# Optimization experiments

Hardware: AMD Instinct MI355X
Metric: run time of the kernel (lower is better)

Reference implementation:

```python
import jax, jax.numpy as jnp
import numpy as np

N_NODES = 50000
N_EDGES = 800000
D_IN = 128
D_HID = 128
D_OUT = 128


def _gcn_layer(x, W, b, src, dst, norm):
    # dense projection then edge-weighted gather -> scatter-add at dst
    h = x @ W                                   # [N, d_out]
    msg = h[src] * norm[:, None]                # [E, d_out]
    out = jax.ops.segment_sum(msg, dst, num_segments=N_NODES)
    return out + b


def setup_inputs() -> dict:
    key = jax.random.key(0)
    k = jax.random.split(key, 8)
    x = jax.random.normal(k[0], (N_NODES, D_IN), dtype=jnp.float32)
    edge_index = jax.random.randint(k[1], (2, N_EDGES), 0, N_NODES, dtype=jnp.int64)
    edge_weight = jax.random.uniform(k[2], (N_EDGES,), dtype=jnp.float32)
    # GCNConv params (glorot-ish scale)
    s1 = 1.0 / np.sqrt(D_IN)
    s2 = 1.0 / np.sqrt(D_HID)
    W1 = jax.random.normal(k[3], (D_IN, D_HID), dtype=jnp.float32) * s1
    b1 = jnp.zeros((D_HID,), dtype=jnp.float32)
    W2 = jax.random.normal(k[4], (D_HID, D_OUT), dtype=jnp.float32) * s2
    b2 = jnp.zeros((D_OUT,), dtype=jnp.float32)
    return {"x": x, "edge_index": edge_index, "edge_weight": edge_weight,
            "W1": W1, "b1": b1, "W2": W2, "b2": b2}


def reference(x, edge_index, edge_weight, W1, b1, W2, b2):
    src, dst = edge_index[0], edge_index[1]
    # gcn_norm (add_self_loops=False): deg from scatter-add of edge_weight at dst
    deg = jax.ops.segment_sum(edge_weight, dst, num_segments=N_NODES)
    dinv = jnp.where(deg > 0, jax.lax.rsqrt(jnp.maximum(deg, 1e-30)), 0.0)
    norm = dinv[src] * edge_weight * dinv[dst]  # [E]
    h = jax.nn.relu(_gcn_layer(x, W1, b1, src, dst, norm))
    out = _gcn_layer(h, W2, b2, src, dst, norm)
    # F.dropout in eval mode (deterministic reference) is identity
    return out
```

## Files before the change

### kernel.cpp

```cpp
#include <hip/hip_runtime.h>

#define N_NODES 50000
#define N_EDGES 800000
#define D 128
#define MAXDEG 64
#define NBUCK 196
#define BUCKCAP 5120
#define EPB 4096
#define NBB 196
#define SP 136

typedef __attribute__((ext_vector_type(8))) short bf16x8;
typedef __attribute__((ext_vector_type(4))) float f32x4;

__device__ inline unsigned short f2bf(float f) {
    unsigned u = __float_as_uint(f);
    unsigned r = (u + 0x7fffu + ((u >> 16) & 1u)) >> 16;
    return (unsigned short)r;
}

__global__ __launch_bounds__(256) void k_bucket(const int* __restrict__ src,
                                                const int* __restrict__ dst,
                                                const float* __restrict__ ew,
                                                int* __restrict__ cursor,
                                                uint2* __restrict__ buck,
                                                const float* __restrict__ W1,
                                                const float* __restrict__ W2,
                                                unsigned short* __restrict__ Wt1,
                                                unsigned short* __restrict__ Wt2) {
    if (blockIdx.x >= NBB) {
        const float* W = (blockIdx.x == NBB) ? W1 : W2;
        unsigned short* Wt = (blockIdx.x == NBB) ? Wt1 : Wt2;
        for (int idx = threadIdx.x; idx < D * D; idx += 256) {
            int n = idx & 127, k = idx >> 7;
            Wt[n * D + k] = f2bf(W[k * D + n]);
        }
        return;
    }
    __shared__ uint2 sorted[EPB];
    __shared__ int hist[NBUCK];
    __shared__ int scn[NBUCK];
    __shared__ int gbase[NBUCK];
    __shared__ int s[256];
    int tid = threadIdx.x;
    int e0 = blockIdx.x * EPB;
    for (int i = tid; i < NBUCK; i += 256) hist[i] = 0;
    __syncthreads();
    #pragma unroll
    for (int j = 0; j < 16; ++j) {
        int e = e0 + j * 256 + tid;
        if (e < N_EDGES) atomicAdd(&hist[dst[e] >> 8], 1);
    }
    __syncthreads();
    int v = tid < NBUCK ? hist[tid] : 0;
    s[tid] = v;
    __syncthreads();
    for (int off = 1; off < 256; off <<= 1) {
        int u = tid >= off ? s[tid - off] : 0;
        __syncthreads();
        s[tid] += u;
        __syncthreads();
    }
    int excl = s[tid] - v;
    if (tid < NBUCK) {
        scn[tid] = excl;
        gbase[tid] = v ? atomicAdd(&cursor[tid], v) : 0;
        hist[tid] = excl;
    }
    __syncthreads();
    #pragma unroll
    for (int j = 0; j < 16; ++j) {
        int e = e0 + j * 256 + tid;
        if (e < N_EDGES) {
            int d = dst[e];
            int sv = src[e];
            unsigned wf = min(__float2uint_rn(ew[e] * 65536.f), 65535u);
            int slot = atomicAdd(&hist[d >> 8], 1);
            sorted[slot] = make_uint2(((unsigned)sv << 16) | wf, (unsigned)d);
        }
    }
    __syncthreads();
    int total = min(EPB, N_EDGES - e0);
    for (int i = tid; i < total; i += 256) {
        uint2 en = sorted[i];
        int bk = (int)(en.y >> 8);
        int g = gbase[bk] + (i - scn[bk]);
        if (g < BUCKCAP)
            buck[(size_t)bk * BUCKCAP + g] = make_uint2(en.x, en.y & 255u);
    }
}

#define GB 782
__global__ __launch_bounds__(256) void k_build_gemm(
        const int* __restrict__ cursor, const uint2* __restrict__ buck,
        unsigned* __restrict__ csr, int* __restrict__ cnt,
        float* __restrict__ dinv,
        const float* __restrict__ X, const unsigned short* __restrict__ Wt1,
        unsigned short* __restrict__ h0) {
    __shared__ union SM {
        struct {
            unsigned csr_loc[256 * MAXDEG];
            int cnt_loc[256];
            int deg_loc[256];
        } b;
        unsigned short sX[64 * D];
    } sm;
    int tid = threadIdx.x;

    if (blockIdx.x < NBUCK) {
        int b = blockIdx.x;
        sm.b.cnt_loc[tid] = 0;
        sm.b.deg_loc[tid] = 0;
        {
            uint4* z4 = (uint4*)sm.b.csr_loc;
            #pragma unroll
            for (int i = 0; i < (256 * MAXDEG / 4) / 256; ++i)
                z4[i * 256 + tid] = make_uint4(0u, 0u, 0u, 0u);
        }
        __syncthreads();
        int n = min(cursor[b], BUCKCAP);
        const uint2* bb = buck + (size_t)b * BUCKCAP;
        for (int i = tid; i < n; i += 256) {
            uint2 e = bb[i];
            int ln = e.y;
            int slot = atomicAdd(&sm.b.cnt_loc[ln], 1);
            if (slot < MAXDEG) sm.b.csr_loc[ln * MAXDEG + slot] = e.x;
            atomicAdd(&sm.b.deg_loc[ln], (int)(e.x & 0xffffu));
        }
        __syncthreads();
        int node0 = b * 256;
        int nnodes = min(256, N_NODES - node0);
        uint4* g = (uint4*)(csr + (size_t)node0 * MAXDEG);
        const uint4* l = (const uint4*)sm.b.csr_loc;
        int nv = nnodes * (MAXDEG / 4);
        for (int i = tid; i < nv; i += 256) g[i] = l[i];
        if (tid < nnodes) {
            int node = node0 + tid;
            cnt[node] = min(sm.b.cnt_loc[tid], MAXDEG);
            float sum = (float)sm.b.deg_loc[tid] * (1.f / 65536.f);
            dinv[node] = sum > 0.f ? rsqrtf(fmaxf(sum, 1e-30f)) : 0.f;
        }
        return;
    }

    int row0 = (blockIdx.x - NBUCK) * 64;
    int nr = min(64, N_NODES - row0);
    {
        const float4* xs = (const float4*)(X + (size_t)row0 * D);
        int nvec = nr * (D / 4);
        for (int i = tid; i < nvec; i += 256) {
            float4 v = xs[i];
            ushort4 o;
            o.x = f2bf(v.x); o.y = f2bf(v.y); o.z = f2bf(v.z); o.w = f2bf(v.w);
            *(ushort4*)(sm.sX + i * 4) = o;
        }
    }
    __syncthreads();

    int wave = tid >> 6, lane = tid & 63;
    int m = lane & 15, quad = lane >> 4;
    f32x4 acc[8];
    #pragma unroll
    for (int i = 0; i < 8; ++i) acc[i] = (f32x4){0.f, 0.f, 0.f, 0.f};

    const unsigned short* aBase = sm.sX + (wave * 16 + m) * D + quad * 8;
    #pragma unroll
    for (int c = 0; c < 4; ++c) {
        bf16x8 a = *(const bf16x8*)(aBase + c * 32);
        #pragma unroll
        for (int n0 = 0; n0 < 8; ++n0) {
            bf16x8 b = *(const bf16x8*)(Wt1 + (n0 * 16 + m) * D + c * 32 + quad * 8);
            acc[n0] = __builtin_amdgcn_mfma_f32_16x16x32_bf16(a, b, acc[n0], 0, 0, 0);
        }
    }

    unsigned short* sOut = sm.sX + wave * 16 * D;
    __syncthreads();
    #pragma unroll
    for (int n0 = 0; n0 < 8; ++n0)
        #pragma unroll
        for (int i = 0; i < 4; ++i)
            sOut[(quad * 4 + i) * D + n0 * 16 + m] = f2bf(acc[n0][i]);
    __syncthreads();
    int rr = lane >> 2, c0 = (lane & 3) * 32;
    int grow = row0 + wave * 16 + rr;
    if (grow < N_NODES) {
        uint4* dstp = (uint4*)(h0 + (size_t)grow * D + c0);
        const uint4* srcp = (const uint4*)(sOut + rr * D + c0);
        dstp[0] = srcp[0]; dstp[1] = srcp[1]; dstp[2] = srcp[2]; dstp[3] = srcp[3];
    }
}

__global__ __launch_bounds__(256) void k_agg_mm(const unsigned short* __restrict__ H,
                                                const int* __restrict__ cnt,
                                                const unsigned* __restrict__ csr,
                                                const float* __restrict__ dinv,
                                                const float* __restrict__ b1,
                                                const unsigned short* __restrict__ Wt2,
                                                unsigned short* __restrict__ Hb) {
    __shared__ unsigned short sT[16 * SP];
    int tid = threadIdx.x, wave = tid >> 6, lane = tid & 63;
    int g = lane >> 4, fl = lane & 15;
    int nb = blockIdx.x * 16;
    int node = nb + wave * 4 + g;

    int end = min(cnt[node], MAXDEG);
    const uint4* row4 = (const uint4*)(csr + (size_t)node * MAXDEG);
    float acc[8] = {0.f, 0.f, 0.f, 0.f, 0.f, 0.f, 0.f, 0.f};
    for (int b0 = 0; b0 < end; b0 += 8) {
        uint4 ca = row4[(b0 >> 2)];
        uint4 cb = row4[(b0 >> 2) + 1];
        unsigned cs[8] = {ca.x, ca.y, ca.z, ca.w, cb.x, cb.y, cb.z, cb.w};
        uint4 u[8];
        float nmv[8];
        #pragma unroll
        for (int j = 0; j < 8; ++j) {
            unsigned sv = cs[j] >> 16;
            u[j] = *(const uint4*)(H + (size_t)sv * D + fl * 8);
            nmv[j] = (float)(cs[j] & 0xffffu) * (1.f / 65536.f) * dinv[sv];
        }
        #pragma unroll
        for (int j = 0; j < 8; ++j) {
            unsigned a0[4] = {u[j].x, u[j].y, u[j].z, u[j].w};
            #pragma unroll
            for (int q = 0; q < 4; ++q) {
                acc[2 * q]     += __uint_as_float(a0[q] << 16) * nmv[j];
                acc[2 * q + 1] += __uint_as_float(a0[q] & 0xffff0000u) * nmv[j];
            }
        }
    }
    {
        float dn = dinv[node];
        int f = fl * 8;
        float4 bv0 = *(const float4*)(b1 + f);
        float4 bv1 = *(const float4*)(b1 + f + 4);
        ushort4 o0, o1;
        o0.x = f2bf(fmaxf(acc[0] * dn + bv0.x, 0.f));
        o0.y = f2bf(fmaxf(acc[1] * dn + bv0.y, 0.f));
        o0.z = f2bf(fmaxf(acc[2] * dn + bv0.z, 0.f));
        o0.w = f2bf(fmaxf(acc[3] * dn + bv0.w, 0.f));
        o1.x = f2bf(fmaxf(acc[4] * dn + bv1.x, 0.f));
        o1.y = f2bf(fmaxf(acc[5] * dn + bv1.y, 0.f));
        o1.z = f2bf(fmaxf(acc[6] * dn + bv1.z, 0.f));
        o1.w = f2bf(fmaxf(acc[7] * dn + bv1.w, 0.f));
        unsigned short* tp = sT + (wave * 4 + g) * SP + f;
        *(ushort4*)(tp) = o0;
        *(ushort4*)(tp + 4) = o1;
    }
    __syncthreads();

    int m = lane & 15, quad = lane >> 4;
    f32x4 acc2[2];
    acc2[0] = (f32x4){0.f, 0.f, 0.f, 0.f};
    acc2[1] = (f32x4){0.f, 0.f, 0.f, 0.f};
    #pragma unroll
    for (int c = 0; c < 4; ++c) {
        bf16x8 a = *(const bf16x8*)(sT + m * SP + c * 32 + quad * 8);
        #pragma unroll
        for (int t = 0; t < 2; ++t) {
            int n0 = wave * 2 + t;
            bf16x8 b = *(const bf16x8*)(Wt2 + (n0 * 16 + m) * D + c * 32 + quad * 8);
            acc2[t] = __builtin_amdgcn_mfma_f32_16x16x32_bf16(a, b, acc2[t], 0, 0, 0);
        }
    }
    float dv[4];
    #pragma unroll
    for (int i = 0; i < 4; ++i) dv[i] = dinv[nb + quad * 4 + i];
    __syncthreads();
    #pragma unroll
    for (int t = 0; t < 2; ++t)
        #pragma unroll
        for (int i = 0; i < 4; ++i)
            sT[(quad * 4 + i) * SP + (wave * 2 + t) * 16 + m] = f2bf(acc2[t][i] * dv[i]);
    __syncthreads();
    int rr = tid >> 4, cc = (tid & 15) * 8;
    *(uint4*)(Hb + (size_t)(nb + rr) * D + cc) = *(const uint4*)(sT + rr * SP + cc);
}

__global__ __launch_bounds__(256) void k_aggregate(const unsigned short* __restrict__ H,
                                                   const int* __restrict__ cnt,
                                                   const unsigned* __restrict__ csr,
                                                   const float* __restrict__ dinv,
                                                   const float* __restrict__ bias,
                                                   float* __restrict__ out) {
    int tid = threadIdx.x, wave = tid >> 6, lane = tid & 63;
    int g = lane >> 4, fl = lane & 15;
    int node = blockIdx.x * 16 + wave * 4 + g;

    int end = min(cnt[node], MAXDEG);
    const uint4* row4 = (const uint4*)(csr + (size_t)node * MAXDEG);
    float acc[8] = {0.f, 0.f, 0.f, 0.f, 0.f, 0.f, 0.f, 0.f};
    for (int b0 = 0; b0 < end; b0 += 8) {
        uint4 ca = row4[(b0 >> 2)];
        uint4 cb = row4[(b0 >> 2) + 1];
        unsigned cs[8] = {ca.x, ca.y, ca.z, ca.w, cb.x, cb.y, cb.z, cb.w};
        uint4 u[8];
        float nmv[8];
        #pragma unroll
        for (int j = 0; j < 8; ++j) {
            unsigned sv = cs[j] >> 16;
            u[j] = *(const uint4*)(H + (size_t)sv * D + fl * 8);
            nmv[j] = (float)(cs[j] & 0xffffu) * (1.f / 65536.f);
        }
        #pragma unroll
        for (int j = 0; j < 8; ++j) {
            unsigned a0[4] = {u[j].x, u[j].y, u[j].z, u[j].w};
            #pragma unroll
            for (int q = 0; q < 4; ++q) {
                acc[2 * q]     += __uint_as_float(a0[q] << 16) * nmv[j];
                acc[2 * q + 1] += __uint_as_float(a0[q] & 0xffff0000u) * nmv[j];
            }
        }
    }
    float dn = dinv[node];
    int f = fl * 8;
    float4 bv0 = *(const float4*)(bias + f);
    float4 bv1 = *(const float4*)(bias + f + 4);
    float* op = out + (size_t)node * D + f;
    *(float4*)(op) = make_float4(acc[0] * dn + bv0.x, acc[1] * dn + bv0.y,
                                 acc[2] * dn + bv0.z, acc[3] * dn + bv0.w);
    *(float4*)(op + 4) = make_float4(acc[4] * dn + bv1.x, acc[5] * dn + bv1.y,
                                     acc[6] * dn + bv1.z, acc[7] * dn + bv1.w);
}

extern "C" void kernel_launch(void* const* d_in, const int* in_sizes, int n_in,
                              void* d_out, int out_size, void* d_ws, size_t ws_size,
                              hipStream_t stream) {
    const float* x   = (const float*)d_in[0];
    const int*   ei  = (const int*)d_in[1];
    const float* ew  = (const float*)d_in[2];
    const float* W1  = (const float*)d_in[3];
    const float* b1  = (const float*)d_in[4];
    const float* W2  = (const float*)d_in[5];
    const float* b2  = (const float*)d_in[6];
    float* out = (float*)d_out;

    const int* src = ei;
    const int* dst = ei + N_EDGES;

    char* base = (char*)d_ws;
    size_t off = 0;
    auto take = [&](size_t bytes) -> char* {
        char* p = base + off;
        off += (bytes + 255) & ~(size_t)255;
        return p;
    };
    int*      cursor = (int*)take(NBUCK * 4);
    size_t zero_bytes = off;
    float*    dinv = (float*)take(N_NODES * 4);
    int*      cnt  = (int*)take(N_NODES * 4);
    uint2*    buck = (uint2*)take((size_t)NBUCK * BUCKCAP * 8);
    unsigned* csr  = (unsigned*)take((size_t)N_NODES * MAXDEG * 4);
    unsigned short* Wt1 = (unsigned short*)take(D * D * 2);
    unsigned short* Wt2 = (unsigned short*)take(D * D * 2);
    unsigned short* h0  = (unsigned short*)take((size_t)N_NODES * D * 2);
    unsigned short* hb  = (unsigned short*)take((size_t)N_NODES * D * 2);

    hipMemsetAsync(d_ws, 0, zero_bytes, stream);

    const int FB = N_NODES / 16;
    const int AB = N_NODES / 16;

    k_bucket<<<NBB + 2, 256, 0, stream>>>(src, dst, ew, cursor, buck,
                                          W1, W2, Wt1, Wt2);
    k_build_gemm<<<NBUCK + GB, 256, 0, stream>>>(cursor, buck, csr, cnt, dinv,
                                                 x, Wt1, h0);
    k_agg_mm<<<FB, 256, 0, stream>>>(h0, cnt, csr, dinv, b1, Wt2, hb);
    k_aggregate<<<AB, 256, 0, stream>>>(hb, cnt, csr, dinv, b2, out);
}
```

Before: 194.9 us.

## Replace two-pass bucket sort CSR build with direct global-atomic CSR insertion

Drops the shared-memory bucket sort and the per-bucket build pass. Each edge now inserts itself into the padded CSR with global atomics on cnt and deg. The memset is replaced by a zeroing kernel that also does the weight transposes, and dinv is computed from the integer degree inside the consumers rather than stored. This removes one intermediate buffer pass and the bucket scratch, but puts many scattered global atomics and uncoalesced CSR writes in its place, and it must zero the whole CSR region (about 12.8MB) every call.

```diff
diff --git a/kernel.cpp b/kernel.cpp
--- a/kernel.cpp
+++ b/kernel.cpp
@@ -4,11 +4,11 @@
 #define N_EDGES 800000
 #define D 128
 #define MAXDEG 64
-#define NBUCK 196
-#define BUCKCAP 5120
-#define EPB 4096
-#define NBB 196
 #define SP 136
+
+#define EB 391
+#define GB 782
+#define PZB 200
 
 typedef __attribute__((ext_vector_type(8))) short bf16x8;
 typedef __attribute__((ext_vector_type(4))) float f32x4;
@@ -19,131 +19,68 @@
     return (unsigned short)r;
 }
 
-__global__ __launch_bounds__(256) void k_bucket(const int* __restrict__ src,
-                                                const int* __restrict__ dst,
-                                                const float* __restrict__ ew,
-                                                int* __restrict__ cursor,
-                                                uint2* __restrict__ buck,
-                                                const float* __restrict__ W1,
-                                                const float* __restrict__ W2,
-                                                unsigned short* __restrict__ Wt1,
-                                                unsigned short* __restrict__ Wt2) {
-    if (blockIdx.x >= NBB) {
-        const float* W = (blockIdx.x == NBB) ? W1 : W2;
-        unsigned short* Wt = (blockIdx.x == NBB) ? Wt1 : Wt2;
-        for (int idx = threadIdx.x; idx < D * D; idx += 256) {
+__device__ inline float deg2dinv(int di) {
+    return di > 0 ? rsqrtf((float)di * (1.f / 65536.f)) : 0.f;
+}
+
+__global__ __launch_bounds__(256) void k_prep(const float* __restrict__ W1,
+                                              const float* __restrict__ W2,
+                                              unsigned short* __restrict__ Wt1,
+                                              unsigned short* __restrict__ Wt2,
+                                              uint4* __restrict__ zbase,
+                                              int nz4) {
+    int tid = threadIdx.x;
+    if (blockIdx.x < 2) {
+        const float* W = (blockIdx.x == 0) ? W1 : W2;
+        unsigned short* Wt = (blockIdx.x == 0) ? Wt1 : Wt2;
+        for (int idx = tid; idx < D * D; idx += 256) {
             int n = idx & 127, k = idx >> 7;
             Wt[n * D + k] = f2bf(W[k * D + n]);
         }
         return;
     }
-    __shared__ uint2 sorted[EPB];
-    __shared__ int hist[NBUCK];
-    __shared__ int scn[NBUCK];
-    __shared__ int gbase[NBUCK];
-    __shared__ int s[256];
-    int tid = threadIdx.x;
-    int e0 = blockIdx.x * EPB;
-    for (int i = tid; i < NBUCK; i += 256) hist[i] = 0;
-    __syncthreads();
-    #pragma unroll
-    for (int j = 0; j < 16; ++j) {
-        int e = e0 + j * 256 + tid;
-        if (e < N_EDGES) atomicAdd(&hist[dst[e] >> 8], 1);
-    }
-    __syncthreads();
-    int v = tid < NBUCK ? hist[tid] : 0;
-    s[tid] = v;
-    __syncthreads();
-    for (int off = 1; off < 256; off <<= 1) {
-        int u = tid >= off ? s[tid - off] : 0;
-        __syncthreads();
-        s[tid] += u;
-        __syncthreads();
-    }
-    int excl = s[tid] - v;
-    if (tid < NBUCK) {
-        scn[tid] = excl;
-        gbase[tid] = v ? atomicAdd(&cursor[tid], v) : 0;
-        hist[tid] = excl;
-    }
-    __syncthreads();
-    #pragma unroll
-    for (int j = 0; j < 16; ++j) {
-        int e = e0 + j * 256 + tid;
-        if (e < N_EDGES) {
-            int d = dst[e];
-            int sv = src[e];
-            unsigned wf = min(__float2uint_rn(ew[e] * 65536.f), 65535u);
-            int slot = atomicAdd(&hist[d >> 8], 1);
-            sorted[slot] = make_uint2(((unsigned)sv << 16) | wf, (unsigned)d);
-        }
-    }
-    __syncthreads();
-    int total = min(EPB, N_EDGES - e0);
-    for (int i = tid; i < total; i += 256) {
-        uint2 en = sorted[i];
-        int bk = (int)(en.y >> 8);
-        int g = gbase[bk] + (i - scn[bk]);
-        if (g < BUCKCAP)
-            buck[(size_t)bk * BUCKCAP + g] = make_uint2(en.x, en.y & 255u);
-    }
-}
-
-#define GB 782
-__global__ __launch_bounds__(256) void k_build_gemm(
-        const int* __restrict__ cursor, const uint2* __restrict__ buck,
-        unsigned* __restrict__ csr, int* __restrict__ cnt,
-        float* __restrict__ dinv,
+    for (int i = (blockIdx.x - 2) * 256 + tid; i < nz4; i += PZB * 256)
+        zbase[i] = make_uint4(0u, 0u, 0u, 0u);
+}
+
+__global__ __launch_bounds__(256) void k_csr_gemm(
+        const int* __restrict__ src, const int* __restrict__ dst,
+        const float* __restrict__ ew,
+        int* __restrict__ cnt, int* __restrict__ deg,
+        unsigned* __restrict__ csr,
         const float* __restrict__ X, const unsigned short* __restrict__ Wt1,
         unsigned short* __restrict__ h0) {
-    __shared__ union SM {
-        struct {
-            unsigned csr_loc[256 * MAXDEG];
-            int cnt_loc[256];
-            int deg_loc[256];
-        } b;
-        unsigned short sX[64 * D];
-    } sm;
+    __shared__ unsigned short sX[64 * D];
     int tid = threadIdx.x;
 
-    if (blockIdx.x < NBUCK) {
-        int b = blockIdx.x;
-        sm.b.cnt_loc[tid] = 0;
-        sm.b.deg_loc[tid] = 0;
-        {
-            uint4* z4 = (uint4*)sm.b.csr_loc;
-            #pragma unroll
-            for (int i = 0; i < (256 * MAXDEG / 4) / 256; ++i)
-                z4[i * 256 + tid] = make_uint4(0u, 0u, 0u, 0u);
-        }
-        __syncthreads();
-        int n = min(cursor[b], BUCKCAP);
-        const uint2* bb = buck + (size_t)b * BUCKCAP;
-        for (int i = tid; i < n; i += 256) {
-            uint2 e = bb[i];
-            int ln = e.y;
-            int slot = atomicAdd(&sm.b.cnt_loc[ln], 1);
-            if (slot < MAXDEG) sm.b.csr_loc[ln * MAXDEG + slot] = e.x;
-            atomicAdd(&sm.b.deg_loc[ln], (int)(e.x & 0xffffu));
-        }
-        __syncthreads();
-        int node0 = b * 256;
-        int nnodes = min(256, N_NODES - node0);
-        uint4* g = (uint4*)(csr + (size_t)node0 * MAXDEG);
-        const uint4* l = (const uint4*)sm.b.csr_loc;
-        int nv = nnodes * (MAXDEG / 4);
-        for (int i = tid; i < nv; i += 256) g[i] = l[i];
-        if (tid < nnodes) {
-            int node = node0 + tid;
-            cnt[node] = min(sm.b.cnt_loc[tid], MAXDEG);
-            float sum = (float)sm.b.deg_loc[tid] * (1.f / 65536.f);
-            dinv[node] = sum > 0.f ? rsqrtf(fmaxf(sum, 1e-30f)) : 0.f;
+    if (blockIdx.x < EB) {
+        int e0 = blockIdx.x * 2048;
+        int d8[8];
+        unsigned p8[8];
+        #pragma unroll
+        for (int j = 0; j < 8; ++j) {
+            int e = e0 + j * 256 + tid;
+            if (e < N_EDGES) {
+                d8[j] = dst[e];
+                unsigned wf = min(__float2uint_rn(ew[e] * 65536.f), 65535u);
+                p8[j] = ((unsigned)src[e] << 16) | wf;
+            } else {
+                d8[j] = -1;
+            }
+        }
+        #pragma unroll
+        for (int j = 0; j < 8; ++j) {
+            if (d8[j] >= 0) {
+                int slot = atomicAdd(&cnt[d8[j]], 1);
+                if (slot < MAXDEG)
+                    csr[(size_t)d8[j] * MAXDEG + slot] = p8[j];
+                atomicAdd(&deg[d8[j]], (int)(p8[j] & 0xffffu));
+            }
         }
         return;
     }
 
-    int row0 = (blockIdx.x - NBUCK) * 64;
+    int row0 = (blockIdx.x - EB) * 64;
     int nr = min(64, N_NODES - row0);
     {
         const float4* xs = (const float4*)(X + (size_t)row0 * D);
@@ -152,7 +89,7 @@
             float4 v = xs[i];
             ushort4 o;
             o.x = f2bf(v.x); o.y = f2bf(v.y); o.z = f2bf(v.z); o.w = f2bf(v.w);
-            *(ushort4*)(sm.sX + i * 4) = o;
+            *(ushort4*)(sX + i * 4) = o;
         }
     }
     __syncthreads();
@@ -163,7 +100,7 @@
     #pragma unroll
     for (int i = 0; i < 8; ++i) acc[i] = (f32x4){0.f, 0.f, 0.f, 0.f};
 
-    const unsigned short* aBase = sm.sX + (wave * 16 + m) * D + quad * 8;
+    const unsigned short* aBase = sX + (wave * 16 + m) * D + quad * 8;
     #pragma unroll
     for (int c = 0; c < 4; ++c) {
         bf16x8 a = *(const bf16x8*)(aBase + c * 32);
@@ -174,7 +111,7 @@
         }
     }
 
-    unsigned short* sOut = sm.sX + wave * 16 * D;
+    unsigned short* sOut = sX + wave * 16 * D;
     __syncthreads();
     #pragma unroll
     for (int n0 = 0; n0 < 8; ++n0)
@@ -194,7 +131,7 @@
 __global__ __launch_bounds__(256) void k_agg_mm(const unsigned short* __restrict__ H,
                                                 const int* __restrict__ cnt,
                                                 const unsigned* __restrict__ csr,
-                                                const float* __restrict__ dinv,
+                                                const int* __restrict__ deg,
                                                 const float* __restrict__ b1,
                                                 const unsigned short* __restrict__ Wt2,
                                                 unsigned short* __restrict__ Hb) {
@@ -217,7 +154,8 @@
         for (int j = 0; j < 8; ++j) {
             unsigned sv = cs[j] >> 16;
             u[j] = *(const uint4*)(H + (size_t)sv * D + fl * 8);
-            nmv[j] = (float)(cs[j] & 0xffffu) * (1.f / 65536.f) * dinv[sv];
+            nmv[j] = (float)(cs[j] & 0xffffu) * (1.f / 65536.f)
+                     * deg2dinv(deg[sv]);
         }
         #pragma unroll
         for (int j = 0; j < 8; ++j) {
@@ -230,7 +168,7 @@
         }
     }
     {
-        float dn = dinv[node];
+        float dn = deg2dinv(deg[node]);
         int f = fl * 8;
         float4 bv0 = *(const float4*)(b1 + f);
         float4 bv1 = *(const float4*)(b1 + f + 4);
@@ -265,7 +203,7 @@
     }
     float dv[4];
     #pragma unroll
-    for (int i = 0; i < 4; ++i) dv[i] = dinv[nb + quad * 4 + i];
+    for (int i = 0; i < 4; ++i) dv[i] = deg2dinv(deg[nb + quad * 4 + i]);
     __syncthreads();
     #pragma unroll
     for (int t = 0; t < 2; ++t)
@@ -280,7 +218,7 @@
 __global__ __launch_bounds__(256) void k_aggregate(const unsigned short* __restrict__ H,
                                                    const int* __restrict__ cnt,
                                                    const unsigned* __restrict__ csr,
-                                                   const float* __restrict__ dinv,
+                                                   const int* __restrict__ deg,
                                                    const float* __restrict__ bias,
                                                    float* __restrict__ out) {
     int tid = threadIdx.x, wave = tid >> 6, lane = tid & 63;
@@ -312,7 +250,7 @@
             }
         }
     }
-    float dn = dinv[node];
+    float dn = deg2dinv(deg[node]);
     int f = fl * 8;
     float4 bv0 = *(const float4*)(bias + f);
     float4 bv1 = *(const float4*)(bias + f + 4);
@@ -345,26 +283,24 @@
         off += (bytes + 255) & ~(size_t)255;
         return p;
     };
-    int*      cursor = (int*)take(NBUCK * 4);
-    size_t zero_bytes = off;
-    float*    dinv = (float*)take(N_NODES * 4);
-    int*      cnt  = (int*)take(N_NODES * 4);
-    uint2*    buck = (uint2*)take((size_t)NBUCK * BUCKCAP * 8);
-    unsigned* csr  = (unsigned*)take((size_t)N_NODES * MAXDEG * 4);
+    size_t z0 = off;
+    int*      cnt = (int*)take(N_NODES * 4);
+    int*      deg = (int*)take(N_NODES * 4);
+    unsigned* csr = (unsigned*)take((size_t)N_NODES * MAXDEG * 4);
+    size_t z1 = off;
     unsigned short* Wt1 = (unsigned short*)take(D * D * 2);
     unsigned short* Wt2 = (unsigned short*)take(D * D * 2);
     unsigned short* h0  = (unsigned short*)take((size_t)N_NODES * D * 2);
     unsigned short* hb  = (unsigned short*)take((size_t)N_NODES * D * 2);
 
-    hipMemsetAsync(d_ws, 0, zero_bytes, stream);
+    int nz4 = (int)((z1 - z0) / 16);
 
     const int FB = N_NODES / 16;
-    const int AB = N_NODES / 16;
-
-    k_bucket<<<NBB + 2, 256, 0, stream>>>(src, dst, ew, cursor, buck,
-                                          W1, W2, Wt1, Wt2);
-    k_build_gemm<<<NBUCK + GB, 256, 0, stream>>>(cursor, buck, csr, cnt, dinv,
-                                                 x, Wt1, h0);
-    k_agg_mm<<<FB, 256, 0, stream>>>(h0, cnt, csr, dinv, b1, Wt2, hb);
-    k_aggregate<<<AB, 256, 0, stream>>>(hb, cnt, csr, dinv, b2, out);
-}
+
+    k_prep<<<2 + PZB, 256, 0, stream>>>(W1, W2, Wt1, Wt2,
+                                        (uint4*)(base + z0), nz4);
+    k_csr_gemm<<<EB + GB, 256, 0, stream>>>(src, dst, ew, cnt, deg, csr,
+                                            x, Wt1, h0);
+    k_agg_mm<<<FB, 256, 0, stream>>>(h0, cnt, csr, deg, b1, Wt2, hb);
+    k_aggregate<<<FB, 256, 0, stream>>>(hb, cnt, csr, deg, b2, out);
+}
```

After: 271.3 us. +39.2%, slower.

## Compute degrees globally in bucketing and fold source dinv into GEMM output

Applied to the files above, without the earlier changes.

Degrees are now accumulated with global atomics during the bucketing pass, so dinv can be computed before the first GEMM. The source-side dinv scale is applied to the projected rows instead of being gathered per edge in the aggregation loop. The bucketing pass uses smaller edge chunks (more blocks), and the CSR build splits each 256-node bucket across two blocks, each filtering to its half. The costs are global atomic contention on deg, each half-bucket block reading the full bucket, and an extra deg read in the GEMM epilogue.

```diff
diff --git a/kernel.cpp b/kernel.cpp
--- a/kernel.cpp
+++ b/kernel.cpp
@@ -6,8 +6,10 @@
 #define MAXDEG 64
 #define NBUCK 196
 #define BUCKCAP 5120
-#define EPB 4096
-#define NBB 196
+#define EPB 2048
+#define NBB 391
+#define NB2 392
+#define GB 782
 #define SP 136
 
 typedef __attribute__((ext_vector_type(8))) short bf16x8;
@@ -19,10 +21,15 @@
     return (unsigned short)r;
 }
 
+__device__ inline float deg2dinv(int di) {
+    return di > 0 ? rsqrtf((float)di * (1.f / 65536.f)) : 0.f;
+}
+
 __global__ __launch_bounds__(256) void k_bucket(const int* __restrict__ src,
                                                 const int* __restrict__ dst,
                                                 const float* __restrict__ ew,
                                                 int* __restrict__ cursor,
+                                                int* __restrict__ deg,
                                                 uint2* __restrict__ buck,
                                                 const float* __restrict__ W1,
                                                 const float* __restrict__ W2,
@@ -47,7 +54,7 @@
     for (int i = tid; i < NBUCK; i += 256) hist[i] = 0;
     __syncthreads();
     #pragma unroll
-    for (int j = 0; j < 16; ++j) {
+    for (int j = 0; j < EPB / 256; ++j) {
         int e = e0 + j * 256 + tid;
         if (e < N_EDGES) atomicAdd(&hist[dst[e] >> 8], 1);
     }
@@ -69,12 +76,13 @@
     }
     __syncthreads();
     #pragma unroll
-    for (int j = 0; j < 16; ++j) {
+    for (int j = 0; j < EPB / 256; ++j) {
         int e = e0 + j * 256 + tid;
         if (e < N_EDGES) {
             int d = dst[e];
             int sv = src[e];
             unsigned wf = min(__float2uint_rn(ew[e] * 65536.f), 65535u);
+            atomicAdd(&deg[d], (int)wf);
             int slot = atomicAdd(&hist[d >> 8], 1);
             sorted[slot] = make_uint2(((unsigned)sv << 16) | wf, (unsigned)d);
         }
@@ -90,60 +98,61 @@
     }
 }
 
-#define GB 782
 __global__ __launch_bounds__(256) void k_build_gemm(
         const int* __restrict__ cursor, const uint2* __restrict__ buck,
         unsigned* __restrict__ csr, int* __restrict__ cnt,
-        float* __restrict__ dinv,
+        float* __restrict__ dinv, const int* __restrict__ deg,
         const float* __restrict__ X, const unsigned short* __restrict__ Wt1,
         unsigned short* __restrict__ h0) {
     __shared__ union SM {
         struct {
-            unsigned csr_loc[256 * MAXDEG];
-            int cnt_loc[256];
-            int deg_loc[256];
+            unsigned csr_loc[128 * MAXDEG];
+            int cnt_loc[128];
         } b;
         unsigned short sX[64 * D];
     } sm;
     int tid = threadIdx.x;
 
-    if (blockIdx.x < NBUCK) {
+    if (blockIdx.x < NB2) {
         int b = blockIdx.x;
-        sm.b.cnt_loc[tid] = 0;
-        sm.b.deg_loc[tid] = 0;
+        int bucket = b >> 1;
+        unsigned hbit = (unsigned)(b & 1) << 7;
+        if (tid < 128) sm.b.cnt_loc[tid] = 0;
         {
             uint4* z4 = (uint4*)sm.b.csr_loc;
             #pragma unroll
-            for (int i = 0; i < (256 * MAXDEG / 4) / 256; ++i)
+            for (int i = 0; i < (128 * MAXDEG / 4) / 256; ++i)
                 z4[i * 256 + tid] = make_uint4(0u, 0u, 0u, 0u);
         }
         __syncthreads();
-        int n = min(cursor[b], BUCKCAP);
-        const uint2* bb = buck + (size_t)b * BUCKCAP;
+        int n = min(cursor[bucket], BUCKCAP);
+        const uint2* bb = buck + (size_t)bucket * BUCKCAP;
         for (int i = tid; i < n; i += 256) {
             uint2 e = bb[i];
-            int ln = e.y;
-            int slot = atomicAdd(&sm.b.cnt_loc[ln], 1);
-            if (slot < MAXDEG) sm.b.csr_loc[ln * MAXDEG + slot] = e.x;
-            atomicAdd(&sm.b.deg_loc[ln], (int)(e.x & 0xffffu));
+            if ((e.y & 128u) == hbit) {
+                int ln = (int)(e.y & 127u);
+                int slot = atomicAdd(&sm.b.cnt_loc[ln], 1);
+                if (slot < MAXDEG) sm.b.csr_loc[ln * MAXDEG + slot] = e.x;
+            }
         }
         __syncthreads();
-        int node0 = b * 256;
-        int nnodes = min(256, N_NODES - node0);
-        uint4* g = (uint4*)(csr + (size_t)node0 * MAXDEG);
-        const uint4* l = (const uint4*)sm.b.csr_loc;
-        int nv = nnodes * (MAXDEG / 4);
-        for (int i = tid; i < nv; i += 256) g[i] = l[i];
-        if (tid < nnodes) {
-            int node = node0 + tid;
-            cnt[node] = min(sm.b.cnt_loc[tid], MAXDEG);
-            float sum = (float)sm.b.deg_loc[tid] * (1.f / 65536.f);
-            dinv[node] = sum > 0.f ? rsqrtf(fmaxf(sum, 1e-30f)) : 0.f;
+        int node0 = b * 128;
+        int nnodes = min(128, N_NODES - node0);
+        if (nnodes > 0) {
+            uint4* g = (uint4*)(csr + (size_t)node0 * MAXDEG);
+            const uint4* l = (const uint4*)sm.b.csr_loc;
+            int nv = nnodes * (MAXDEG / 4);
+            for (int i = tid; i < nv; i += 256) g[i] = l[i];
+            if (tid < nnodes) {
+                int node = node0 + tid;
+                cnt[node] = min(sm.b.cnt_loc[tid], MAXDEG);
+                dinv[node] = deg2dinv(deg[node]);
+            }
         }
         return;
     }
 
-    int row0 = (blockIdx.x - NBUCK) * 64;
+    int row0 = (blockIdx.x - NB2) * 64;
     int nr = min(64, N_NODES - row0);
     {
         const float4* xs = (const float4*)(X + (size_t)row0 * D);
@@ -174,13 +183,20 @@
         }
     }
 
+    float dn[4];
+    #pragma unroll
+    for (int i = 0; i < 4; ++i) {
+        int r = row0 + wave * 16 + quad * 4 + i;
+        dn[i] = (r < N_NODES) ? deg2dinv(deg[r]) : 0.f;
+    }
+
     unsigned short* sOut = sm.sX + wave * 16 * D;
     __syncthreads();
     #pragma unroll
     for (int n0 = 0; n0 < 8; ++n0)
         #pragma unroll
         for (int i = 0; i < 4; ++i)
-            sOut[(quad * 4 + i) * D + n0 * 16 + m] = f2bf(acc[n0][i]);
+            sOut[(quad * 4 + i) * D + n0 * 16 + m] = f2bf(acc[n0][i] * dn[i]);
     __syncthreads();
     int rr = lane >> 2, c0 = (lane & 3) * 32;
     int grow = row0 + wave * 16 + rr;
@@ -217,7 +233,7 @@
         for (int j = 0; j < 8; ++j) {
             unsigned sv = cs[j] >> 16;
             u[j] = *(const uint4*)(H + (size_t)sv * D + fl * 8);
-            nmv[j] = (float)(cs[j] & 0xffffu) * (1.f / 65536.f) * dinv[sv];
+            nmv[j] = (float)(cs[j] & 0xffffu) * (1.f / 65536.f);
         }
         #pragma unroll
         for (int j = 0; j < 8; ++j) {
@@ -346,6 +362,7 @@
         return p;
     };
     int*      cursor = (int*)take(NBUCK * 4);
+    int*      deg    = (int*)take(N_NODES * 4);
     size_t zero_bytes = off;
     float*    dinv = (float*)take(N_NODES * 4);
     int*      cnt  = (int*)take(N_NODES * 4);
@@ -359,12 +376,11 @@
     hipMemsetAsync(d_ws, 0, zero_bytes, stream);
 
     const int FB = N_NODES / 16;
-    const int AB = N_NODES / 16;
-
-    k_bucket<<<NBB + 2, 256, 0, stream>>>(src, dst, ew, cursor, buck,
+
+    k_bucket<<<NBB + 2, 256, 0, stream>>>(src, dst, ew, cursor, deg, buck,
                                           W1, W2, Wt1, Wt2);
-    k_build_gemm<<<NBUCK + GB, 256, 0, stream>>>(cursor, buck, csr, cnt, dinv,
-                                                 x, Wt1, h0);
+    k_build_gemm<<<NB2 + GB, 256, 0, stream>>>(cursor, buck, csr, cnt, dinv,
+                                               deg, x, Wt1, h0);
     k_agg_mm<<<FB, 256, 0, stream>>>(h0, cnt, csr, dinv, b1, Wt2, hb);
-    k_aggregate<<<AB, 256, 0, stream>>>(hb, cnt, csr, dinv, b2, out);
-}
+    k_aggregate<<<FB, 256, 0, stream>>>(hb, cnt, csr, dinv, b2, out);
+}
```

New measurement: 234.1 us. +20.2%, slower.
